# Performance work log

Hardware: AMD Instinct MI355X
Metric: run time of the kernel (lower is better)

## Reference

```python
import jax, jax.numpy as jnp
import numpy as np
import math

K_HISTORY = 32  # sliding-window length over GRU hidden states


def rotate_half(x):
    half = x.shape[-1] // 2
    return jnp.concatenate([-x[..., half:], x[..., :half]], axis=-1)


def setup_inputs() -> dict:
    key = jax.random.key(0)
    ks = jax.random.split(key, 8)
    B, MB, IN = 8, 512, 1024          # batch, max_bin, input_size (gru_hidden_size)
    EMB, H, KVH, HD, BS = 1024, 16, 4, 64, 16  # embed_dim, heads, kv_heads, head_dim, bin_size
    h = jax.random.normal(ks[0], (B, MB, IN), jnp.float32)
    # RoPE tables: rotate-half layout, theta repeated over both halves
    pos = jnp.arange(MB, dtype=jnp.float32)
    inv_freq = 1.0 / (10000.0 ** (jnp.arange(0, HD, 2, dtype=jnp.float32) / HD))
    theta = pos[:, None] * inv_freq[None, :]            # (MB, HD/2)
    theta = jnp.concatenate([theta, theta], axis=-1)    # (MB, HD)
    freqs_cos = jnp.cos(theta)
    freqs_sin = jnp.sin(theta)
    s = 0.02
    Wq = jax.random.normal(ks[1], (EMB, H * HD), jnp.float32) * s
    Wk = jax.random.normal(ks[2], (IN, KVH * HD), jnp.float32) * s
    Wv = jax.random.normal(ks[3], (IN, KVH * HD), jnp.float32) * s
    Wo = jax.random.normal(ks[4], (H * HD, EMB), jnp.float32) * s
    output_queries = jax.random.normal(ks[5], (BS, EMB), jnp.float32)
    Wr = jax.random.normal(ks[6], (EMB, 2), jnp.float32) * s
    br = jnp.zeros((2,), jnp.float32)
    return {"h": h, "freqs_cos": freqs_cos, "freqs_sin": freqs_sin,
            "Wq": Wq, "Wk": Wk, "Wv": Wv, "Wo": Wo,
            "output_queries": output_queries, "Wr": Wr, "br": br}


def reference(h, freqs_cos, freqs_sin, Wq, Wk, Wv, Wo, output_queries, Wr, br):
    B, MB, IN = h.shape
    HD = freqs_cos.shape[1]
    H = Wq.shape[1] // HD
    KVH = Wk.shape[1] // HD
    n_rep = H // KVH
    BS = output_queries.shape[0]
    K = K_HISTORY

    # sliding windows over bins: window t covers h[t-K+1 : t+1] (zero left-pad)
    h_padded = jnp.concatenate([jnp.zeros((B, K - 1, IN), h.dtype), h], axis=1)
    idx = jnp.arange(MB)[:, None] + jnp.arange(K)[None, :]   # (MB, K)
    h_win = h_padded[:, idx, :]                              # (B, MB, K, IN)

    k = (h_win @ Wk).reshape(B, MB, K, KVH, HD)
    v = (h_win @ Wv).reshape(B, MB, K, KVH, HD)

    # queries: shared learned output queries, identical across batch & bins
    q = (output_queries @ Wq).reshape(BS, H, HD)             # (BS, H, HD)
    # RoPE on Q only (is_decoder=True) at within-bin offsets 0..BS-1
    offs = jnp.arange(BS)
    cos = freqs_cos[offs][:, None, :]                        # (BS, 1, HD)
    sin = freqs_sin[offs][:, None, :]
    q = q * cos + rotate_half(q) * sin                       # (BS, H, HD)

    # GQA: repeat_interleave KV heads to H heads
    k = jnp.repeat(k, n_rep, axis=3)                         # (B, MB, K, H, HD)
    v = jnp.repeat(v, n_rep, axis=3)

    scores = jnp.einsum("qhd,bmkhd->bmhqk", q, k) / math.sqrt(HD)
    attn = jax.nn.softmax(scores, axis=-1)                   # (B, MB, H, BS, K)
    attn_out = jnp.einsum("bmhqk,bmkhd->bmqhd", attn, v)
    attn_out = attn_out.reshape(B, MB, BS, H * HD)

    z = attn_out @ Wo                                        # (B, MB, BS, EMB)
    vel = z @ Wr + br                                        # (B, MB, BS, 2)
    return vel.reshape(B, MB * BS, 2)
```

## Files before the change

kernel.cpp:

```cpp
#include <hip/hip_runtime.h>


typedef __attribute__((ext_vector_type(8))) short v8s;
typedef __attribute__((ext_vector_type(4))) float v4f;

#define OFF_WOR  0u
#define OFF_QR   2048u
#define OFF_WTH  18432u
#define OFF_WTL  182272u
#define OFF_S0   346112u
#define OFF_S1   1460224u
#define OFF_VW0  2574336u
#define OFF_VW1  2713600u
#define OFF_AH   2852864u
#define OFF_AL   4950016u
#define SROW 544

__device__ __forceinline__ void split_bf16(float a, unsigned short& h, unsigned short& l) {
    const unsigned u = __float_as_uint(a);
    h = (unsigned short)(u >> 16);
    const float r = a - __uint_as_float(u & 0xFFFF0000u);
    unsigned v = __float_as_uint(r);
    v += 0x7FFFu + ((v >> 16) & 1u);
    l = (unsigned short)(v >> 16);
}

__global__ __launch_bounds__(256) void kP(
    const float* __restrict__ oq, const float* __restrict__ Wq,
    const float* __restrict__ fc, const float* __restrict__ fs,
    const float* __restrict__ Wo, const float* __restrict__ Wr,
    const float* __restrict__ hsrc,
    float* __restrict__ qr, float* __restrict__ Wor,
    float* __restrict__ S0, float* __restrict__ S1,
    float* __restrict__ VW0, float* __restrict__ VW1,
    unsigned* __restrict__ wthu, unsigned* __restrict__ wtlu,
    unsigned short* __restrict__ Ahg, unsigned short* __restrict__ Alg)
{
    __shared__ float sm[2048];
    const int b = blockIdx.x, t = threadIdx.x;
    if (b >= 658) {
        const int base = (b - 658) * 2048 + t * 8;
        const float4 x0 = *(const float4*)(hsrc + base);
        const float4 x1 = *(const float4*)(hsrc + base + 4);
        const float af[8] = {x0.x, x0.y, x0.z, x0.w, x1.x, x1.y, x1.z, x1.w};
        v8s ah, al;
        #pragma unroll
        for (int j = 0; j < 8; ++j) {
            unsigned short hh, ll;
            split_bf16(af[j], hh, ll);
            ah[j] = (short)hh; al[j] = (short)ll;
        }
        *(v8s*)(Ahg + base) = ah;
        *(v8s*)(Alg + base) = al;
        return;
    }
    if (b < 256) {
        const int q = b >> 4, h = b & 15;
        #pragma unroll
        for (int j = 0; j < 4; ++j) sm[t + 256 * j] = oq[q * 1024 + t + 256 * j];
        __syncthreads();
        const int w = t >> 6, lane = t & 63;
        const float* wq = Wq + (size_t)(w * 256) * 1024 + h * 64 + lane;
        const float* os = sm + w * 256;
        float acc = 0.f;
        #pragma unroll 16
        for (int e = 0; e < 256; ++e) acc = fmaf(os[e], wq[(size_t)e * 1024], acc);
        sm[1024 + w * 64 + lane] = acc;
        __syncthreads();
        if (t < 64) {
            const int d = t, p = d ^ 32;
            const float a1 = sm[1024 + d] + sm[1088 + d] + sm[1152 + d] + sm[1216 + d];
            const float a2 = sm[1024 + p] + sm[1088 + p] + sm[1152 + p] + sm[1216 + p];
            const float c = fc[q * 64 + d], s = fs[q * 64 + d];
            const float rh = (d < 32) ? -a2 : a2;
            qr[q * 1024 + h * 64 + d] = fmaf(a1, c, rh * s);
        }
    } else if (b < 512) {
        #pragma unroll
        for (int j = 0; j < 8; ++j) sm[t + 256 * j] = Wr[t + 256 * j];
        __syncthreads();
        const int i = (b - 256) * 4 + (t >> 6);
        const int lane = t & 63;
        float a0 = 0.f, a1 = 0.f;
        const float* wo = Wo + (size_t)i * 1024 + lane;
        #pragma unroll
        for (int j = 0; j < 16; ++j) {
            const float w = wo[j * 64];
            const int e = lane + j * 64;
            a0 = fmaf(w, sm[2 * e], a0);
            a1 = fmaf(w, sm[2 * e + 1], a1);
        }
        #pragma unroll
        for (int w = 1; w < 64; w <<= 1) {
            a0 += __shfl_xor(a0, w, 64);
            a1 += __shfl_xor(a1, w, 64);
        }
        if (lane == 0) { Wor[i * 2] = a0; Wor[i * 2 + 1] = a1; }
    } else if (b < 656) {
        const int idx = (b - 512) * 256 + t;
        const float4 z = make_float4(0.f, 0.f, 0.f, 0.f);
        if (idx < 16384)       *(float4*)(S0  + (size_t)(idx >> 3) * SROW + (idx & 7) * 4) = z;
        else if (idx < 32768)  *(float4*)(S1  + (size_t)((idx - 16384) >> 3) * SROW + (idx & 7) * 4) = z;
        else if (idx < 34816)  *(float4*)(VW0 + (size_t)((idx - 32768) >> 3) * SROW + (idx & 7) * 4) = z;
        else                   *(float4*)(VW1 + (size_t)((idx - 34816) >> 3) * SROW + (idx & 7) * 4) = z;
    } else {
        unsigned* dst = (b == 656) ? wthu : wtlu;
        #pragma unroll
        for (int j = 0; j < 64; ++j) dst[147456 + t + 256 * j] = 0u;
    }
}

__global__ __launch_bounds__(256) void kW(
    const float* __restrict__ Wk, const float* __restrict__ Wv,
    const float* __restrict__ qr, const float* __restrict__ Wor,
    unsigned short* __restrict__ Wth, unsigned short* __restrict__ Wtl)
{
    __shared__ float As[16 * 68];
    __shared__ float Bt[72 * 68];
    const int b = blockIdx.x, t = threadIdx.x;
    const int g = b & 3, i0 = (b >> 2) * 16;
    #pragma unroll
    for (int jj = 0; jj < 16; ++jj) {
        const int i2 = t + 256 * jj;
        const int d = i2 & 63, col = i2 >> 6;
        Bt[col * 68 + d] = qr[(col >> 2) * 1024 + (g * 4 + (col & 3)) * 64 + d];
    }
    #pragma unroll
    for (int jj = 0; jj < 2; ++jj) {
        const int i2 = t + 256 * jj;
        const int d = i2 & 63, vc = i2 >> 6;
        Bt[(64 + vc) * 68 + d] = Wor[((g * 4 + (vc >> 1)) * 64 + d) * 2 + (vc & 1)];
    }
    {
        const int i = t >> 4, dc = (t & 15) * 4;
        *(float4*)&As[i * 68 + dc] = *(const float4*)(Wk + (size_t)(i0 + i) * 256 + g * 64 + dc);
    }
    __syncthreads();
    const int jc = t & 63, iq = t >> 6;
    {
        float o4[4] = {0.f, 0.f, 0.f, 0.f};
        #pragma unroll
        for (int dc = 0; dc < 16; ++dc) {
            const float4 bv = *(const float4*)&Bt[jc * 68 + dc * 4];
            #pragma unroll
            for (int r = 0; r < 4; ++r) {
                const float4 av = *(const float4*)&As[(iq * 4 + r) * 68 + dc * 4];
                o4[r] = fmaf(av.x, bv.x, o4[r]);
                o4[r] = fmaf(av.y, bv.y, o4[r]);
                o4[r] = fmaf(av.z, bv.z, o4[r]);
                o4[r] = fmaf(av.w, bv.w, o4[r]);
            }
        }
        const int j = (jc >> 2) * 16 + g * 4 + (jc & 3);
        #pragma unroll
        for (int r = 0; r < 4; ++r) {
            unsigned short hh, ll;
            split_bf16(o4[r] * 0.125f, hh, ll);
            Wth[(size_t)j * 1024 + i0 + iq * 4 + r] = hh;
            Wtl[(size_t)j * 1024 + i0 + iq * 4 + r] = ll;
        }
    }
    __syncthreads();
    {
        const int i = t >> 4, dc = (t & 15) * 4;
        *(float4*)&As[i * 68 + dc] = *(const float4*)(Wv + (size_t)(i0 + i) * 256 + g * 64 + dc);
    }
    __syncthreads();
    if (t < 128) {
        const int il = t >> 3, vc = t & 7;
        float acc = 0.f;
        #pragma unroll
        for (int dc = 0; dc < 16; ++dc) {
            const float4 av = *(const float4*)&As[il * 68 + dc * 4];
            const float4 bv = *(const float4*)&Bt[(64 + vc) * 68 + dc * 4];
            acc = fmaf(av.x, bv.x, acc);
            acc = fmaf(av.y, bv.y, acc);
            acc = fmaf(av.z, bv.z, acc);
            acc = fmaf(av.w, bv.w, acc);
        }
        const int j = 256 + (g * 4 + (vc >> 1)) * 2 + (vc & 1);
        unsigned short hh, ll;
        split_bf16(acc, hh, ll);
        Wth[(size_t)j * 1024 + i0 + il] = hh;
        Wtl[(size_t)j * 1024 + i0 + il] = ll;
    }
}

__global__ __launch_bounds__(256) void k2(
    const unsigned short* __restrict__ Ahg, const unsigned short* __restrict__ Alg,
    const unsigned short* __restrict__ Wth, const unsigned short* __restrict__ Wtl,
    float* __restrict__ S0, float* __restrict__ S1,
    float* __restrict__ VW0, float* __restrict__ VW1)
{
    __shared__ unsigned short Ah[64 * 72], Al[64 * 72];
    __shared__ unsigned short Bh[64 * 72], Bl[64 * 72];
    const int m0 = blockIdx.x * 64;
    const int n0 = blockIdx.y * 64;
    const int kh = blockIdx.z;
    const int t = threadIdx.x;
    const int lane = t & 63, wv = t >> 6;
    const int l16 = lane & 15, quad = lane >> 4;
    const int wm = wv >> 1, wn = wv & 1;
    const int sr = t >> 2, kc = (t & 3) * 8;
    v4f acc[2][2];
    #pragma unroll
    for (int i = 0; i < 2; ++i)
        #pragma unroll
        for (int j = 0; j < 2; ++j) acc[i][j] = (v4f)(0.f);
    const unsigned short* Aph = Ahg + (size_t)(m0 + sr) * 1024 + kh * 512 + kc;
    const unsigned short* Apl = Alg + (size_t)(m0 + sr) * 1024 + kh * 512 + kc;
    const unsigned short* Bph = Wth + (size_t)(n0 + sr) * 1024 + kh * 512 + kc;
    const unsigned short* Bpl = Wtl + (size_t)(n0 + sr) * 1024 + kh * 512 + kc;
    v8s rah0 = *(const v8s*)(Aph);      v8s rah1 = *(const v8s*)(Aph + 32);
    v8s ral0 = *(const v8s*)(Apl);      v8s ral1 = *(const v8s*)(Apl + 32);
    v8s rbh0 = *(const v8s*)(Bph);      v8s rbh1 = *(const v8s*)(Bph + 32);
    v8s rbl0 = *(const v8s*)(Bpl);      v8s rbl1 = *(const v8s*)(Bpl + 32);
    for (int k0 = 0; k0 < 512; k0 += 64) {
        __syncthreads();
        *(v8s*)&Ah[sr * 72 + kc] = rah0;  *(v8s*)&Ah[sr * 72 + kc + 32] = rah1;
        *(v8s*)&Al[sr * 72 + kc] = ral0;  *(v8s*)&Al[sr * 72 + kc + 32] = ral1;
        *(v8s*)&Bh[sr * 72 + kc] = rbh0;  *(v8s*)&Bh[sr * 72 + kc + 32] = rbh1;
        *(v8s*)&Bl[sr * 72 + kc] = rbl0;  *(v8s*)&Bl[sr * 72 + kc + 32] = rbl1;
        __syncthreads();
        if (k0 + 64 < 512) {
            const int kn = k0 + 64;
            rah0 = *(const v8s*)(Aph + kn);  rah1 = *(const v8s*)(Aph + kn + 32);
            ral0 = *(const v8s*)(Apl + kn);  ral1 = *(const v8s*)(Apl + kn + 32);
            rbh0 = *(const v8s*)(Bph + kn);  rbh1 = *(const v8s*)(Bph + kn + 32);
            rbl0 = *(const v8s*)(Bpl + kn);  rbl1 = *(const v8s*)(Bpl + kn + 32);
        }
        #pragma unroll
        for (int kk = 0; kk < 2; ++kk) {
            v8s fah[2], fal[2], fbh[2], fbl[2];
            #pragma unroll
            for (int s = 0; s < 2; ++s) {
                const int mr = wm * 32 + s * 16 + l16;
                fah[s] = *(const v8s*)&Ah[mr * 72 + kk * 32 + quad * 8];
                fal[s] = *(const v8s*)&Al[mr * 72 + kk * 32 + quad * 8];
                const int nr = wn * 32 + s * 16 + l16;
                fbh[s] = *(const v8s*)&Bh[nr * 72 + kk * 32 + quad * 8];
                fbl[s] = *(const v8s*)&Bl[nr * 72 + kk * 32 + quad * 8];
            }
            #pragma unroll
            for (int ms = 0; ms < 2; ++ms)
                #pragma unroll
                for (int ns = 0; ns < 2; ++ns) {
                    acc[ms][ns] = __builtin_amdgcn_mfma_f32_16x16x32_bf16(fal[ms], fbh[ns], acc[ms][ns], 0, 0, 0);
                    acc[ms][ns] = __builtin_amdgcn_mfma_f32_16x16x32_bf16(fah[ms], fbl[ns], acc[ms][ns], 0, 0, 0);
                    acc[ms][ns] = __builtin_amdgcn_mfma_f32_16x16x32_bf16(fah[ms], fbh[ns], acc[ms][ns], 0, 0, 0);
                }
        }
    }
    float* Sh  = kh ? S1 : S0;
    float* VWh = kh ? VW1 : VW0;
    #pragma unroll
    for (int ms = 0; ms < 2; ++ms)
        #pragma unroll
        for (int ns = 0; ns < 2; ++ns) {
            const int j = n0 + wn * 32 + ns * 16 + l16;
            if (j >= 288) continue;
            const int m = m0 + wm * 32 + ms * 16 + quad * 4;
            const int bb = m >> 9, tt = m & 511;
            const float4 v = make_float4(acc[ms][ns][0], acc[ms][ns][1], acc[ms][ns][2], acc[ms][ns][3]);
            float* dst;
            if (j < 256)
                dst = Sh + (size_t)((bb * 16 + (j >> 4)) * 16 + (j & 15)) * SROW + 32 + tt;
            else
                dst = VWh + (size_t)(bb * 32 + (j - 256)) * SROW + 32 + tt;
            *(float4*)dst = v;
        }
}

__global__ __launch_bounds__(256) void k3(
    const float* __restrict__ S0, const float* __restrict__ S1,
    const float* __restrict__ VW0, const float* __restrict__ VW1,
    const float* __restrict__ brp, float* __restrict__ out)
{
    __shared__ float Es[16 * 164];
    __shared__ float EVs[32 * 164];
    const int b = blockIdx.x, q = blockIdx.y, qt = blockIdx.z;
    const int tbase = qt * 128;
    const int t = threadIdx.x;
    for (int idx = t; idx < 640; idx += 256) {
        const int h = idx / 40, g = idx - h * 40;
        const size_t off = (size_t)((b * 16 + q) * 16 + h) * SROW + tbase + g * 4;
        const float4 a = *(const float4*)(S0 + off);
        const float4 c = *(const float4*)(S1 + off);
        float4 e;
        e.x = __expf(a.x + c.x); e.y = __expf(a.y + c.y);
        e.z = __expf(a.z + c.z); e.w = __expf(a.w + c.w);
        *(float4*)(Es + h * 164 + g * 4) = e;
    }
    __syncthreads();
    for (int idx = t; idx < 1280; idx += 256) {
        const int hc = idx / 40, g = idx - hc * 40;
        const size_t off = (size_t)(b * 32 + hc) * SROW + tbase + g * 4;
        const float4 v0 = *(const float4*)(VW0 + off);
        const float4 v1 = *(const float4*)(VW1 + off);
        const float4 e = *(const float4*)(Es + (hc >> 1) * 164 + g * 4);
        float4 rr;
        rr.x = e.x * (v0.x + v1.x); rr.y = e.y * (v0.y + v1.y);
        rr.z = e.z * (v0.z + v1.z); rr.w = e.w * (v0.w + v1.w);
        *(float4*)(EVs + hc * 164 + g * 4) = rr;
    }
    __syncthreads();
    const int h = t & 15, mg = t >> 4;
    const float* ep = Es + h * 164 + mg * 8;
    const float* e0 = EVs + (2 * h) * 164 + mg * 8;
    const float* e1 = EVs + (2 * h + 1) * 164 + mg * 8;
    float den = 0.f, n0s = 0.f, n1s = 0.f;
    #pragma unroll
    for (int s = 0; s < 32; ++s) {
        const int ss = 1 + ((s + 2 * h) & 31);
        den += ep[ss]; n0s += e0[ss]; n1s += e1[ss];
    }
    const float br0 = brp[0], br1 = brp[1];
    #pragma unroll
    for (int u = 0; u < 8; ++u) {
        const float inv = __builtin_amdgcn_rcpf(den);
        float c0 = n0s * inv, c1 = n1s * inv;
        #pragma unroll
        for (int w = 1; w < 16; w <<= 1) {
            c0 += __shfl_xor(c0, w, 64);
            c1 += __shfl_xor(c1, w, 64);
        }
        if (h == 0) {
            const int m = tbase + mg * 8 + u;
            float* o = out + (size_t)((b * 512 + m) * 16 + q) * 2;
            o[0] = c0 + br0;
            o[1] = c1 + br1;
        }
        if (u < 7) {
            den += ep[33 + u] - ep[1 + u];
            n0s += e0[33 + u] - e0[1 + u];
            n1s += e1[33 + u] - e1[1 + u];
        }
    }
}

extern "C" void kernel_launch(void* const* d_in, const int* in_sizes, int n_in,
                              void* d_out, int out_size, void* d_ws, size_t ws_size,
                              hipStream_t stream)
{
    (void)in_sizes; (void)n_in; (void)out_size; (void)ws_size;
    const float* h  = (const float*)d_in[0];
    const float* fc = (const float*)d_in[1];
    const float* fs = (const float*)d_in[2];
    const float* Wq = (const float*)d_in[3];
    const float* Wk = (const float*)d_in[4];
    const float* Wv = (const float*)d_in[5];
    const float* Wo = (const float*)d_in[6];
    const float* oq = (const float*)d_in[7];
    const float* Wr = (const float*)d_in[8];
    const float* br = (const float*)d_in[9];
    float* ws = (float*)d_ws;
    float* Wor  = ws + OFF_WOR;
    float* qr   = ws + OFF_QR;
    unsigned short* Wth = (unsigned short*)(ws + OFF_WTH);
    unsigned short* Wtl = (unsigned short*)(ws + OFF_WTL);
    float* S0   = ws + OFF_S0;
    float* S1   = ws + OFF_S1;
    float* VW0  = ws + OFF_VW0;
    float* VW1  = ws + OFF_VW1;
    unsigned short* Ahg = (unsigned short*)(ws + OFF_AH);
    unsigned short* Alg = (unsigned short*)(ws + OFF_AL);
    float* out = (float*)d_out;

    hipLaunchKernelGGL(kP, dim3(2706), dim3(256), 0, stream,
                       oq, Wq, fc, fs, Wo, Wr, h, qr, Wor, S0, S1, VW0, VW1,
                       (unsigned*)Wth, (unsigned*)Wtl, Ahg, Alg);
    hipLaunchKernelGGL(kW, dim3(256), dim3(256), 0, stream, Wk, Wv, qr, Wor, Wth, Wtl);
    hipLaunchKernelGGL(k2, dim3(64, 5, 2), dim3(256), 0, stream, Ahg, Alg, Wth, Wtl, S0, S1, VW0, VW1);
    hipLaunchKernelGGL(k3, dim3(8, 16, 4), dim3(256), 0, stream, S0, S1, VW0, VW1, br, out);
}
```

Measured before the change: 121.3 us.

## Replace split-K GEMM with in-block K-split reduction and direct global fragment loads

The k2 GEMM no longer splits K across two grid blocks writing separate S0/S1 and VW0/VW1 partial buffers. Each block now splits K across its four waves, loads MFMA fragments straight from global memory with register double-buffering instead of staging through LDS, and reduces the partial sums through shared memory. This removes the second partial buffers, their zeroing in kP and the extra loads and adds in k3. In exchange the grid is halved to 320 blocks, and the uncoalesced-looking direct global loads plus a 4x4 accumulator tile raise register pressure.

```diff
diff --git a/kernel.cpp b/kernel.cpp
--- a/kernel.cpp
+++ b/kernel.cpp
@@ -9,9 +9,7 @@
 #define OFF_WTH  18432u
 #define OFF_WTL  182272u
 #define OFF_S0   346112u
-#define OFF_S1   1460224u
 #define OFF_VW0  2574336u
-#define OFF_VW1  2713600u
 #define OFF_AH   2852864u
 #define OFF_AL   4950016u
 #define SROW 544
@@ -31,15 +29,14 @@
     const float* __restrict__ Wo, const float* __restrict__ Wr,
     const float* __restrict__ hsrc,
     float* __restrict__ qr, float* __restrict__ Wor,
-    float* __restrict__ S0, float* __restrict__ S1,
-    float* __restrict__ VW0, float* __restrict__ VW1,
+    float* __restrict__ S0, float* __restrict__ VW0,
     unsigned* __restrict__ wthu, unsigned* __restrict__ wtlu,
     unsigned short* __restrict__ Ahg, unsigned short* __restrict__ Alg)
 {
     __shared__ float sm[2048];
     const int b = blockIdx.x, t = threadIdx.x;
-    if (b >= 658) {
-        const int base = (b - 658) * 2048 + t * 8;
+    if (b >= 586) {
+        const int base = (b - 586) * 2048 + t * 8;
         const float4 x0 = *(const float4*)(hsrc + base);
         const float4 x1 = *(const float4*)(hsrc + base + 4);
         const float af[8] = {x0.x, x0.y, x0.z, x0.w, x1.x, x1.y, x1.z, x1.w};
@@ -96,15 +93,13 @@
             a1 += __shfl_xor(a1, w, 64);
         }
         if (lane == 0) { Wor[i * 2] = a0; Wor[i * 2 + 1] = a1; }
-    } else if (b < 656) {
+    } else if (b < 584) {
         const int idx = (b - 512) * 256 + t;
         const float4 z = make_float4(0.f, 0.f, 0.f, 0.f);
-        if (idx < 16384)       *(float4*)(S0  + (size_t)(idx >> 3) * SROW + (idx & 7) * 4) = z;
-        else if (idx < 32768)  *(float4*)(S1  + (size_t)((idx - 16384) >> 3) * SROW + (idx & 7) * 4) = z;
-        else if (idx < 34816)  *(float4*)(VW0 + (size_t)((idx - 32768) >> 3) * SROW + (idx & 7) * 4) = z;
-        else                   *(float4*)(VW1 + (size_t)((idx - 34816) >> 3) * SROW + (idx & 7) * 4) = z;
+        if (idx < 16384)  *(float4*)(S0  + (size_t)(idx >> 3) * SROW + (idx & 7) * 4) = z;
+        else              *(float4*)(VW0 + (size_t)((idx - 16384) >> 3) * SROW + (idx & 7) * 4) = z;
     } else {
-        unsigned* dst = (b == 656) ? wthu : wtlu;
+        unsigned* dst = (b == 584) ? wthu : wtlu;
         #pragma unroll
         for (int j = 0; j < 64; ++j) dst[147456 + t + 256 * j] = 0u;
     }
@@ -186,94 +181,89 @@
     }
 }
 
-__global__ __launch_bounds__(256) void k2(
+__global__ __launch_bounds__(256, 2) void k2(
     const unsigned short* __restrict__ Ahg, const unsigned short* __restrict__ Alg,
     const unsigned short* __restrict__ Wth, const unsigned short* __restrict__ Wtl,
-    float* __restrict__ S0, float* __restrict__ S1,
-    float* __restrict__ VW0, float* __restrict__ VW1)
-{
-    __shared__ unsigned short Ah[64 * 72], Al[64 * 72];
-    __shared__ unsigned short Bh[64 * 72], Bl[64 * 72];
+    float* __restrict__ S0, float* __restrict__ VW0)
+{
+    __shared__ float red[4][64][68];
     const int m0 = blockIdx.x * 64;
     const int n0 = blockIdx.y * 64;
-    const int kh = blockIdx.z;
     const int t = threadIdx.x;
-    const int lane = t & 63, wv = t >> 6;
+    const int w = t >> 6, lane = t & 63;
     const int l16 = lane & 15, quad = lane >> 4;
-    const int wm = wv >> 1, wn = wv & 1;
-    const int sr = t >> 2, kc = (t & 3) * 8;
-    v4f acc[2][2];
-    #pragma unroll
-    for (int i = 0; i < 2; ++i)
-        #pragma unroll
-        for (int j = 0; j < 2; ++j) acc[i][j] = (v4f)(0.f);
-    const unsigned short* Aph = Ahg + (size_t)(m0 + sr) * 1024 + kh * 512 + kc;
-    const unsigned short* Apl = Alg + (size_t)(m0 + sr) * 1024 + kh * 512 + kc;
-    const unsigned short* Bph = Wth + (size_t)(n0 + sr) * 1024 + kh * 512 + kc;
-    const unsigned short* Bpl = Wtl + (size_t)(n0 + sr) * 1024 + kh * 512 + kc;
-    v8s rah0 = *(const v8s*)(Aph);      v8s rah1 = *(const v8s*)(Aph + 32);
-    v8s ral0 = *(const v8s*)(Apl);      v8s ral1 = *(const v8s*)(Apl + 32);
-    v8s rbh0 = *(const v8s*)(Bph);      v8s rbh1 = *(const v8s*)(Bph + 32);
-    v8s rbl0 = *(const v8s*)(Bpl);      v8s rbl1 = *(const v8s*)(Bpl + 32);
-    for (int k0 = 0; k0 < 512; k0 += 64) {
-        __syncthreads();
-        *(v8s*)&Ah[sr * 72 + kc] = rah0;  *(v8s*)&Ah[sr * 72 + kc + 32] = rah1;
-        *(v8s*)&Al[sr * 72 + kc] = ral0;  *(v8s*)&Al[sr * 72 + kc + 32] = ral1;
-        *(v8s*)&Bh[sr * 72 + kc] = rbh0;  *(v8s*)&Bh[sr * 72 + kc + 32] = rbh1;
-        *(v8s*)&Bl[sr * 72 + kc] = rbl0;  *(v8s*)&Bl[sr * 72 + kc + 32] = rbl1;
-        __syncthreads();
-        if (k0 + 64 < 512) {
-            const int kn = k0 + 64;
-            rah0 = *(const v8s*)(Aph + kn);  rah1 = *(const v8s*)(Aph + kn + 32);
-            ral0 = *(const v8s*)(Apl + kn);  ral1 = *(const v8s*)(Apl + kn + 32);
-            rbh0 = *(const v8s*)(Bph + kn);  rbh1 = *(const v8s*)(Bph + kn + 32);
-            rbl0 = *(const v8s*)(Bpl + kn);  rbl1 = *(const v8s*)(Bpl + kn + 32);
-        }
-        #pragma unroll
-        for (int kk = 0; kk < 2; ++kk) {
-            v8s fah[2], fal[2], fbh[2], fbl[2];
+
+    const size_t aoff = (size_t)(m0 + l16) * 1024 + w * 256 + quad * 8;
+    const size_t boff = (size_t)(n0 + l16) * 1024 + w * 256 + quad * 8;
+    const unsigned short* pah = Ahg + aoff;
+    const unsigned short* pal = Alg + aoff;
+    const unsigned short* pbh = Wth + boff;
+    const unsigned short* pbl = Wtl + boff;
+
+    v4f acc[4][4];
+    #pragma unroll
+    for (int i = 0; i < 4; ++i)
+        #pragma unroll
+        for (int j = 0; j < 4; ++j) acc[i][j] = (v4f)(0.f);
+
+    v8s fah[2][4], fal[2][4], fbh[2][4], fbl[2][4];
+    #pragma unroll
+    for (int s = 0; s < 4; ++s) {
+        fah[0][s] = *(const v8s*)(pah + s * 16384);
+        fal[0][s] = *(const v8s*)(pal + s * 16384);
+        fbh[0][s] = *(const v8s*)(pbh + s * 16384);
+        fbl[0][s] = *(const v8s*)(pbl + s * 16384);
+    }
+    #pragma unroll 8
+    for (int it = 0; it < 8; ++it) {
+        const int cur = it & 1, nxt = cur ^ 1;
+        if (it < 7) {
+            const int ko = (it + 1) * 32;
             #pragma unroll
-            for (int s = 0; s < 2; ++s) {
-                const int mr = wm * 32 + s * 16 + l16;
-                fah[s] = *(const v8s*)&Ah[mr * 72 + kk * 32 + quad * 8];
-                fal[s] = *(const v8s*)&Al[mr * 72 + kk * 32 + quad * 8];
-                const int nr = wn * 32 + s * 16 + l16;
-                fbh[s] = *(const v8s*)&Bh[nr * 72 + kk * 32 + quad * 8];
-                fbl[s] = *(const v8s*)&Bl[nr * 72 + kk * 32 + quad * 8];
+            for (int s = 0; s < 4; ++s) {
+                fah[nxt][s] = *(const v8s*)(pah + s * 16384 + ko);
+                fal[nxt][s] = *(const v8s*)(pal + s * 16384 + ko);
+                fbh[nxt][s] = *(const v8s*)(pbh + s * 16384 + ko);
+                fbl[nxt][s] = *(const v8s*)(pbl + s * 16384 + ko);
             }
+        }
+        #pragma unroll
+        for (int ms = 0; ms < 4; ++ms)
             #pragma unroll
-            for (int ms = 0; ms < 2; ++ms)
-                #pragma unroll
-                for (int ns = 0; ns < 2; ++ns) {
-                    acc[ms][ns] = __builtin_amdgcn_mfma_f32_16x16x32_bf16(fal[ms], fbh[ns], acc[ms][ns], 0, 0, 0);
-                    acc[ms][ns] = __builtin_amdgcn_mfma_f32_16x16x32_bf16(fah[ms], fbl[ns], acc[ms][ns], 0, 0, 0);
-                    acc[ms][ns] = __builtin_amdgcn_mfma_f32_16x16x32_bf16(fah[ms], fbh[ns], acc[ms][ns], 0, 0, 0);
-                }
-        }
-    }
-    float* Sh  = kh ? S1 : S0;
-    float* VWh = kh ? VW1 : VW0;
-    #pragma unroll
-    for (int ms = 0; ms < 2; ++ms)
-        #pragma unroll
-        for (int ns = 0; ns < 2; ++ns) {
-            const int j = n0 + wn * 32 + ns * 16 + l16;
-            if (j >= 288) continue;
-            const int m = m0 + wm * 32 + ms * 16 + quad * 4;
-            const int bb = m >> 9, tt = m & 511;
-            const float4 v = make_float4(acc[ms][ns][0], acc[ms][ns][1], acc[ms][ns][2], acc[ms][ns][3]);
-            float* dst;
-            if (j < 256)
-                dst = Sh + (size_t)((bb * 16 + (j >> 4)) * 16 + (j & 15)) * SROW + 32 + tt;
-            else
-                dst = VWh + (size_t)(bb * 32 + (j - 256)) * SROW + 32 + tt;
-            *(float4*)dst = v;
-        }
+            for (int ns = 0; ns < 4; ++ns) {
+                acc[ms][ns] = __builtin_amdgcn_mfma_f32_16x16x32_bf16(fal[cur][ms], fbh[cur][ns], acc[ms][ns], 0, 0, 0);
+                acc[ms][ns] = __builtin_amdgcn_mfma_f32_16x16x32_bf16(fah[cur][ms], fbl[cur][ns], acc[ms][ns], 0, 0, 0);
+                acc[ms][ns] = __builtin_amdgcn_mfma_f32_16x16x32_bf16(fah[cur][ms], fbh[cur][ns], acc[ms][ns], 0, 0, 0);
+            }
+    }
+
+    #pragma unroll
+    for (int ms = 0; ms < 4; ++ms)
+        #pragma unroll
+        for (int ns = 0; ns < 4; ++ns)
+            *(v4f*)&red[w][lane][(ms * 4 + ns) * 4] = acc[ms][ns];
+    __syncthreads();
+    #pragma unroll
+    for (int ns = 0; ns < 4; ++ns) {
+        const int j = n0 + ns * 16 + l16;
+        if (j >= 288) continue;
+        const int fo = w * 16 + ns * 4;
+        const v4f s0 = *(const v4f*)&red[0][lane][fo];
+        const v4f s1 = *(const v4f*)&red[1][lane][fo];
+        const v4f s2 = *(const v4f*)&red[2][lane][fo];
+        const v4f s3 = *(const v4f*)&red[3][lane][fo];
+        const v4f sv = s0 + s1 + s2 + s3;
+        const int m = m0 + w * 16 + quad * 4;
+        const int bb = m >> 9, tt = m & 511;
+        float* dst = (j < 256)
+            ? S0  + (size_t)((bb * 16 + (j >> 4)) * 16 + (j & 15)) * SROW + 32 + tt
+            : VW0 + (size_t)(bb * 32 + (j - 256)) * SROW + 32 + tt;
+        *(float4*)dst = make_float4(sv[0], sv[1], sv[2], sv[3]);
+    }
 }
 
 __global__ __launch_bounds__(256) void k3(
-    const float* __restrict__ S0, const float* __restrict__ S1,
-    const float* __restrict__ VW0, const float* __restrict__ VW1,
+    const float* __restrict__ S, const float* __restrict__ VW,
     const float* __restrict__ brp, float* __restrict__ out)
 {
     __shared__ float Es[16 * 164];
@@ -284,23 +274,21 @@
     for (int idx = t; idx < 640; idx += 256) {
         const int h = idx / 40, g = idx - h * 40;
         const size_t off = (size_t)((b * 16 + q) * 16 + h) * SROW + tbase + g * 4;
-        const float4 a = *(const float4*)(S0 + off);
-        const float4 c = *(const float4*)(S1 + off);
+        const float4 a = *(const float4*)(S + off);
         float4 e;
-        e.x = __expf(a.x + c.x); e.y = __expf(a.y + c.y);
-        e.z = __expf(a.z + c.z); e.w = __expf(a.w + c.w);
+        e.x = __expf(a.x); e.y = __expf(a.y);
+        e.z = __expf(a.z); e.w = __expf(a.w);
         *(float4*)(Es + h * 164 + g * 4) = e;
     }
     __syncthreads();
     for (int idx = t; idx < 1280; idx += 256) {
         const int hc = idx / 40, g = idx - hc * 40;
         const size_t off = (size_t)(b * 32 + hc) * SROW + tbase + g * 4;
-        const float4 v0 = *(const float4*)(VW0 + off);
-        const float4 v1 = *(const float4*)(VW1 + off);
+        const float4 v0 = *(const float4*)(VW + off);
         const float4 e = *(const float4*)(Es + (hc >> 1) * 164 + g * 4);
         float4 rr;
-        rr.x = e.x * (v0.x + v1.x); rr.y = e.y * (v0.y + v1.y);
-        rr.z = e.z * (v0.z + v1.z); rr.w = e.w * (v0.w + v1.w);
+        rr.x = e.x * v0.x; rr.y = e.y * v0.y;
+        rr.z = e.z * v0.z; rr.w = e.w * v0.w;
         *(float4*)(EVs + hc * 164 + g * 4) = rr;
     }
     __syncthreads();
@@ -359,17 +347,15 @@
     unsigned short* Wth = (unsigned short*)(ws + OFF_WTH);
     unsigned short* Wtl = (unsigned short*)(ws + OFF_WTL);
     float* S0   = ws + OFF_S0;
-    float* S1   = ws + OFF_S1;
     float* VW0  = ws + OFF_VW0;
-    float* VW1  = ws + OFF_VW1;
     unsigned short* Ahg = (unsigned short*)(ws + OFF_AH);
     unsigned short* Alg = (unsigned short*)(ws + OFF_AL);
     float* out = (float*)d_out;
 
-    hipLaunchKernelGGL(kP, dim3(2706), dim3(256), 0, stream,
-                       oq, Wq, fc, fs, Wo, Wr, h, qr, Wor, S0, S1, VW0, VW1,
+    hipLaunchKernelGGL(kP, dim3(2634), dim3(256), 0, stream,
+                       oq, Wq, fc, fs, Wo, Wr, h, qr, Wor, S0, VW0,
                        (unsigned*)Wth, (unsigned*)Wtl, Ahg, Alg);
     hipLaunchKernelGGL(kW, dim3(256), dim3(256), 0, stream, Wk, Wv, qr, Wor, Wth, Wtl);
-    hipLaunchKernelGGL(k2, dim3(64, 5, 2), dim3(256), 0, stream, Ahg, Alg, Wth, Wtl, S0, S1, VW0, VW1);
-    hipLaunchKernelGGL(k3, dim3(8, 16, 4), dim3(256), 0, stream, S0, S1, VW0, VW1, br, out);
-}
+    hipLaunchKernelGGL(k2, dim3(64, 5), dim3(256), 0, stream, Ahg, Alg, Wth, Wtl, S0, VW0);
+    hipLaunchKernelGGL(k3, dim3(8, 16, 4), dim3(256), 0, stream, S0, VW0, br, out);
+}
```

Measured after the change: 138.1 us. 13.8% more time.
